# Performance work log

Hardware: AMD Instinct MI355X
Metric: run time of the kernel (lower is better)

Reference implementation:

```python
import jax, jax.numpy as jnp
import numpy as np


def setup_inputs() -> dict:
    key = jax.random.key(0)
    kq, kk, kv = jax.random.split(key, 3)
    B, S, D = 16, 4096, 64
    q = jax.random.normal(kq, (B, S, D), dtype=jnp.float32)
    k = jax.random.normal(kk, (B, S, D), dtype=jnp.float32)
    v = jax.random.normal(kv, (B, S, D), dtype=jnp.float32)
    return {"q": q, "k": k, "v": v}


def reference(q, k, v):
    # scale = 1/sqrt(head_dim), the canonical value passed as `scale` in the repo
    scale = 1.0 / jnp.sqrt(jnp.asarray(q.shape[-1], dtype=q.dtype))
    # scores: [B, Sq, Sk] = q @ k^T  (torch.bmm(q, k.transpose(1,2)))
    scores = jnp.einsum("bqd,bkd->bqk", q, k) * scale
    # softmax over key dim (dim=2); dropout p=0.0 is identity in eval
    attention = jax.nn.softmax(scores, axis=2)
    # context: [B, Sq, D] = attention @ v
    context = jnp.einsum("bqk,bkd->bqd", attention, v)
    return (context, attention)
```

## Files before the change

kernel.cpp:

```cpp
#include <hip/hip_runtime.h>
#include <stdint.h>

typedef _Float16 f16x8 __attribute__((ext_vector_type(8)));
typedef _Float16 f16x4 __attribute__((ext_vector_type(4)));
typedef float    f32x4 __attribute__((ext_vector_type(4)));

#define S_LEN 4096
#define D_DIM 64
#define NB 16
constexpr size_t NE = (size_t)NB * S_LEN * D_DIM;

__global__ __launch_bounds__(256) void k_prep3(const float* __restrict__ k,
                                               _Float16* __restrict__ k3) {
  int g = blockIdx.x * 256 + threadIdx.x;
  int tile = g >> 9, c = g & 511;
  int grp = c >> 6, lane = c & 63;
  int ds = grp >> 2, nf = grp & 3;
  int row = nf * 16 + (lane & 15);
  int d0 = ds * 32 + ((lane >> 4) << 3);
  const float* src = k + ((size_t)tile * 64 + row) * D_DIM + d0;
  f32x4 a = *reinterpret_cast<const f32x4*>(src);
  f32x4 b4 = *reinterpret_cast<const f32x4*>(src + 4);
  f16x8 o;
#pragma unroll
  for (int i = 0; i < 4; ++i) {
    o[i] = (_Float16)a[i];
    o[i + 4] = (_Float16)b4[i];
  }
  *reinterpret_cast<f16x8*>(k3 + (size_t)g * 8) = o;
}

__global__ __launch_bounds__(256) void v_prep3(const float* __restrict__ v,
                                               _Float16* __restrict__ v3) {
  __shared__ float t[64][65];
  int tile = blockIdx.x;
  int c = threadIdx.x & 63, rg = threadIdx.x >> 6;
#pragma unroll
  for (int j = 0; j < 16; ++j)
    t[rg + 4 * j][c] = v[((size_t)tile * 64 + rg + 4 * j) * D_DIM + c];
  __syncthreads();
  _Float16* dst = v3 + (size_t)tile * 4096;
#pragma unroll
  for (int j = 0; j < 4; ++j) {
    int cc = threadIdx.x + 256 * j;
    int g = cc >> 6, lane = cc & 63;
    int nf = g >> 2, dn = g & 3;
    int kl = nf * 16 + ((lane >> 4) << 2);
    int d = dn * 16 + (lane & 15);
    f16x4 o;
#pragma unroll
    for (int i = 0; i < 4; ++i) o[i] = (_Float16)t[kl + i][d];
    *reinterpret_cast<f16x4*>(dst + ((g >> 1) << 9) + lane * 8 + ((g & 1) << 2)) = o;
  }
}

constexpr float CEXP = 0.18033688011112042f;

#define PIPE_BARRIER()                                 \
  do {                                                 \
    asm volatile("s_waitcnt lgkmcnt(0)" ::: "memory"); \
    __builtin_amdgcn_s_barrier();                      \
    __builtin_amdgcn_sched_barrier(0);                 \
  } while (0)

__global__ __launch_bounds__(256, 4) void attn_k(const float* __restrict__ q,
                                                 const _Float16* __restrict__ k3,
                                                 const _Float16* __restrict__ v3,
                                                 float* __restrict__ ctx,
                                                 float* __restrict__ att) {
  __shared__ _Float16 ktile[4][4096];
  const int tid = threadIdx.x, w = tid >> 6, lane = tid & 63;
  const int l15 = lane & 15, lh = lane >> 4;
  const int bid = blockIdx.x;
  const int logical = (bid & 7) * 128 + (bid >> 3);
  const int b = logical >> 6, qt = logical & 63;
  const int qrow = qt * 64 + w * 16 + l15;

  f16x8 qf[2];
#pragma unroll
  for (int ds = 0; ds < 2; ++ds) {
    const float* qp = q + ((size_t)b * S_LEN + qrow) * D_DIM + ds * 32 + 8 * lh;
    f32x4 a = *reinterpret_cast<const f32x4*>(qp);
    f32x4 c4 = *reinterpret_cast<const f32x4*>(qp + 4);
#pragma unroll
    for (int i = 0; i < 4; ++i) {
      qf[ds][i] = (_Float16)(a[i] * CEXP);
      qf[ds][i + 4] = (_Float16)(c4[i] * CEXP);
    }
  }

  const _Float16* k3b = k3 + (size_t)(b * 64) * 4096;

  f16x8 s0, s1, s2, s3;
  auto load2 = [&](int ta, int tb2) {
    const _Float16* sa_ = k3b + (size_t)ta * 4096;
    const _Float16* sb_ = k3b + (size_t)tb2 * 4096;
    s0 = *reinterpret_cast<const f16x8*>(sa_ + tid * 8);
    s1 = *reinterpret_cast<const f16x8*>(sa_ + (tid + 256) * 8);
    s2 = *reinterpret_cast<const f16x8*>(sb_ + tid * 8);
    s3 = *reinterpret_cast<const f16x8*>(sb_ + (tid + 256) * 8);
  };
  auto write2 = [&](int set) {
    *reinterpret_cast<f16x8*>(&ktile[set * 2][tid * 8]) = s0;
    *reinterpret_cast<f16x8*>(&ktile[set * 2][(tid + 256) * 8]) = s1;
    *reinterpret_cast<f16x8*>(&ktile[set * 2 + 1][tid * 8]) = s2;
    *reinterpret_cast<f16x8*>(&ktile[set * 2 + 1][(tid + 256) * 8]) = s3;
  };

  auto qk = [&](int buf, f32x4(&sa)[4]) {
#pragma unroll
    for (int ds = 0; ds < 2; ++ds)
#pragma unroll
      for (int nf = 0; nf < 4; ++nf) {
        const int g = ds * 4 + nf;
        f16x8 kf = *reinterpret_cast<const f16x8*>(&ktile[buf][(g * 64 + lane) * 8]);
        sa[nf] = __builtin_amdgcn_mfma_f32_16x16x32_f16(kf, qf[ds], sa[nf], 0, 0, 0);
      }
  };

  const _Float16* v3b = v3 + (size_t)(b * 64) * 4096 + lane * 8;

  load2(0, 1);
  write2(0);
  PIPE_BARRIER();
  load2(2, 3);
  float ls[4] = {};
  f32x4 ca[4] = {};
  for (int p = 0; p < 32; ++p) {
    const int set = p & 1;
    write2(set ^ 1);
    const int na = 2 * p + 4 < 64 ? 2 * p + 4 : 62;
    load2(na, na + 1);
#pragma unroll
    for (int half = 0; half < 2; ++half) {
      const int t = 2 * p + half;
      const _Float16* vp = v3b + (size_t)t * 4096;
      f16x8 vv8[8];
#pragma unroll
      for (int g2 = 0; g2 < 8; ++g2)
        vv8[g2] = *reinterpret_cast<const f16x8*>(vp + (size_t)g2 * 512);
      f32x4 sa[4] = {};
      __builtin_amdgcn_s_setprio(1);
      qk(set * 2 + half, sa);
      __builtin_amdgcn_s_setprio(0);
      f16x4 pb[4];
#pragma unroll
      for (int nf = 0; nf < 4; ++nf) {
        f32x4 pf;
        pf[0] = exp2f(sa[nf][0]);
        pf[1] = exp2f(sa[nf][1]);
        pf[2] = exp2f(sa[nf][2]);
        pf[3] = exp2f(sa[nf][3]);
        ls[nf] += (pf[0] + pf[1]) + (pf[2] + pf[3]);
        pb[nf][0] = (_Float16)pf[0];
        pb[nf][1] = (_Float16)pf[1];
        pb[nf][2] = (_Float16)pf[2];
        pb[nf][3] = (_Float16)pf[3];
      }
      __builtin_amdgcn_s_setprio(1);
#pragma unroll
      for (int nf = 0; nf < 4; ++nf)
#pragma unroll
        for (int dn = 0; dn < 4; ++dn) {
          const int g = nf * 4 + dn;
          f16x4 vf = (g & 1) ? __builtin_shufflevector(vv8[g >> 1], vv8[g >> 1], 4, 5, 6, 7)
                             : __builtin_shufflevector(vv8[g >> 1], vv8[g >> 1], 0, 1, 2, 3);
          ca[dn] = __builtin_amdgcn_mfma_f32_16x16x16f16(vf, pb[nf], ca[dn], 0, 0, 0);
        }
      __builtin_amdgcn_s_setprio(0);
    }
    PIPE_BARRIER();
  }
  float lsum = (ls[0] + ls[1]) + (ls[2] + ls[3]);
  lsum += __shfl_xor(lsum, 16);
  lsum += __shfl_xor(lsum, 32);
  const float linv = 1.0f / lsum;
  const float lb = -__log2f(lsum);

#pragma unroll
  for (int dn = 0; dn < 4; ++dn) {
    f32x4 co = ca[dn];
    co[0] *= linv; co[1] *= linv; co[2] *= linv; co[3] *= linv;
    *reinterpret_cast<f32x4*>(ctx + ((size_t)b * S_LEN + qrow) * D_DIM + dn * 16 + 4 * lh) = co;
  }

  load2(0, 1);
  write2(0);
  PIPE_BARRIER();
  load2(2, 3);
  float* attrow = att + ((size_t)b * S_LEN + qrow) * S_LEN;
  for (int p = 0; p < 32; ++p) {
    const int set = p & 1;
    write2(set ^ 1);
    const int na = 2 * p + 4 < 64 ? 2 * p + 4 : 62;
    load2(na, na + 1);
#pragma unroll
    for (int half = 0; half < 2; ++half) {
      const int t = 2 * p + half;
      f32x4 sa[4] = {};
      __builtin_amdgcn_s_setprio(1);
      qk(set * 2 + half, sa);
      __builtin_amdgcn_s_setprio(0);
#pragma unroll
      for (int nf = 0; nf < 4; ++nf) {
        f32x4 pf;
        pf[0] = exp2f(sa[nf][0] + lb);
        pf[1] = exp2f(sa[nf][1] + lb);
        pf[2] = exp2f(sa[nf][2] + lb);
        pf[3] = exp2f(sa[nf][3] + lb);
        *reinterpret_cast<f32x4*>(attrow + t * 64 + nf * 16 + 4 * lh) = pf;
      }
    }
    PIPE_BARRIER();
  }
}

extern "C" void kernel_launch(void* const* d_in, const int* in_sizes, int n_in,
                              void* d_out, int out_size, void* d_ws, size_t ws_size,
                              hipStream_t stream) {
  const float* q = (const float*)d_in[0];
  const float* k = (const float*)d_in[1];
  const float* v = (const float*)d_in[2];
  float* ctx = (float*)d_out;
  float* att = ctx + NE;

  _Float16* k3 = (_Float16*)d_ws;
  _Float16* v3 = (_Float16*)((char*)d_ws + 2 * NE);

  k_prep3<<<(int)(NE / 8 / 256), 256, 0, stream>>>(k, k3);
  v_prep3<<<NB * 64, 256, 0, stream>>>(v, v3);
  attn_k<<<1024, 256, 0, stream>>>(q, k3, v3, ctx, att);
}
```

Measured before the change: 397.9 us.

## Process two query tiles per block, fusing A's output pass with B's stats pass

Each block now handles 128 query rows as two tiles. The attention-write pass for the first tile is fused with the softmax-sum and PV pass for the second, sharing the K tile loads and barriers. This removes one of four K sweeps per 128 rows. In exchange the grid is halved, launch bounds allow only 2 blocks per CU, and register pressure rises from holding two Q fragments.

```diff
diff --git a/kernel.cpp b/kernel.cpp
--- a/kernel.cpp
+++ b/kernel.cpp
@@ -63,7 +63,7 @@
     __builtin_amdgcn_sched_barrier(0);                 \
   } while (0)
 
-__global__ __launch_bounds__(256, 4) void attn_k(const float* __restrict__ q,
+__global__ __launch_bounds__(256, 2) void attn_k(const float* __restrict__ q,
                                                  const _Float16* __restrict__ k3,
                                                  const _Float16* __restrict__ v3,
                                                  float* __restrict__ ctx,
@@ -72,24 +72,31 @@
   const int tid = threadIdx.x, w = tid >> 6, lane = tid & 63;
   const int l15 = lane & 15, lh = lane >> 4;
   const int bid = blockIdx.x;
-  const int logical = (bid & 7) * 128 + (bid >> 3);
-  const int b = logical >> 6, qt = logical & 63;
-  const int qrow = qt * 64 + w * 16 + l15;
-
-  f16x8 qf[2];
+  const int logical = (bid & 7) * 64 + (bid >> 3);
+  const int b = logical >> 5, pt = logical & 31;
+  const int qrowA = pt * 128 + w * 16 + l15;
+  const int qrowB = qrowA + 64;
+
+  f16x8 qfA[2], qfB[2];
 #pragma unroll
   for (int ds = 0; ds < 2; ++ds) {
-    const float* qp = q + ((size_t)b * S_LEN + qrow) * D_DIM + ds * 32 + 8 * lh;
-    f32x4 a = *reinterpret_cast<const f32x4*>(qp);
-    f32x4 c4 = *reinterpret_cast<const f32x4*>(qp + 4);
+    const float* qpA = q + ((size_t)b * S_LEN + qrowA) * D_DIM + ds * 32 + 8 * lh;
+    const float* qpB = q + ((size_t)b * S_LEN + qrowB) * D_DIM + ds * 32 + 8 * lh;
+    f32x4 a0 = *reinterpret_cast<const f32x4*>(qpA);
+    f32x4 a1 = *reinterpret_cast<const f32x4*>(qpA + 4);
+    f32x4 b0 = *reinterpret_cast<const f32x4*>(qpB);
+    f32x4 b1 = *reinterpret_cast<const f32x4*>(qpB + 4);
 #pragma unroll
     for (int i = 0; i < 4; ++i) {
-      qf[ds][i] = (_Float16)(a[i] * CEXP);
-      qf[ds][i + 4] = (_Float16)(c4[i] * CEXP);
+      qfA[ds][i] = (_Float16)(a0[i] * CEXP);
+      qfA[ds][i + 4] = (_Float16)(a1[i] * CEXP);
+      qfB[ds][i] = (_Float16)(b0[i] * CEXP);
+      qfB[ds][i + 4] = (_Float16)(b1[i] * CEXP);
     }
   }
 
   const _Float16* k3b = k3 + (size_t)(b * 64) * 4096;
+  const _Float16* v3b = v3 + (size_t)(b * 64) * 4096 + lane * 8;
 
   f16x8 s0, s1, s2, s3;
   auto load2 = [&](int ta, int tb2) {
@@ -107,7 +114,7 @@
     *reinterpret_cast<f16x8*>(&ktile[set * 2 + 1][(tid + 256) * 8]) = s3;
   };
 
-  auto qk = [&](int buf, f32x4(&sa)[4]) {
+  auto qk = [&](int buf, const f16x8(&qf)[2], f32x4(&sa)[4]) {
 #pragma unroll
     for (int ds = 0; ds < 2; ++ds)
 #pragma unroll
@@ -118,7 +125,8 @@
       }
   };
 
-  const _Float16* v3b = v3 + (size_t)(b * 64) * 4096 + lane * 8;
+  float* attrowA = att + ((size_t)b * S_LEN + qrowA) * S_LEN;
+  float* attrowB = att + ((size_t)b * S_LEN + qrowB) * S_LEN;
 
   load2(0, 1);
   write2(0);
@@ -141,7 +149,7 @@
         vv8[g2] = *reinterpret_cast<const f16x8*>(vp + (size_t)g2 * 512);
       f32x4 sa[4] = {};
       __builtin_amdgcn_s_setprio(1);
-      qk(set * 2 + half, sa);
+      qk(set * 2 + half, qfA, sa);
       __builtin_amdgcn_s_setprio(0);
       f16x4 pb[4];
 #pragma unroll
@@ -174,21 +182,23 @@
   float lsum = (ls[0] + ls[1]) + (ls[2] + ls[3]);
   lsum += __shfl_xor(lsum, 16);
   lsum += __shfl_xor(lsum, 32);
-  const float linv = 1.0f / lsum;
-  const float lb = -__log2f(lsum);
-
-#pragma unroll
-  for (int dn = 0; dn < 4; ++dn) {
-    f32x4 co = ca[dn];
-    co[0] *= linv; co[1] *= linv; co[2] *= linv; co[3] *= linv;
-    *reinterpret_cast<f32x4*>(ctx + ((size_t)b * S_LEN + qrow) * D_DIM + dn * 16 + 4 * lh) = co;
-  }
+  {
+    const float linv = 1.0f / lsum;
+#pragma unroll
+    for (int dn = 0; dn < 4; ++dn) {
+      f32x4 co = ca[dn];
+      co[0] *= linv; co[1] *= linv; co[2] *= linv; co[3] *= linv;
+      *reinterpret_cast<f32x4*>(ctx + ((size_t)b * S_LEN + qrowA) * D_DIM + dn * 16 + 4 * lh) = co;
+    }
+  }
+  const float lbA = -__log2f(lsum);
 
   load2(0, 1);
   write2(0);
   PIPE_BARRIER();
   load2(2, 3);
-  float* attrow = att + ((size_t)b * S_LEN + qrow) * S_LEN;
+  ls[0] = ls[1] = ls[2] = ls[3] = 0.f;
+  ca[0] = ca[1] = ca[2] = ca[3] = f32x4{};
   for (int p = 0; p < 32; ++p) {
     const int set = p & 1;
     write2(set ^ 1);
@@ -197,18 +207,95 @@
 #pragma unroll
     for (int half = 0; half < 2; ++half) {
       const int t = 2 * p + half;
+      const int buf = set * 2 + half;
+      const _Float16* vp = v3b + (size_t)t * 4096;
+      f16x8 vv8[8];
+#pragma unroll
+      for (int g2 = 0; g2 < 8; ++g2)
+        vv8[g2] = *reinterpret_cast<const f16x8*>(vp + (size_t)g2 * 512);
+      f32x4 saA[4] = {};
+      __builtin_amdgcn_s_setprio(1);
+      qk(buf, qfA, saA);
+      __builtin_amdgcn_s_setprio(0);
+#pragma unroll
+      for (int nf = 0; nf < 4; ++nf) {
+        f32x4 pf;
+        pf[0] = exp2f(saA[nf][0] + lbA);
+        pf[1] = exp2f(saA[nf][1] + lbA);
+        pf[2] = exp2f(saA[nf][2] + lbA);
+        pf[3] = exp2f(saA[nf][3] + lbA);
+        *reinterpret_cast<f32x4*>(attrowA + t * 64 + nf * 16 + 4 * lh) = pf;
+      }
+      f32x4 saB[4] = {};
+      __builtin_amdgcn_s_setprio(1);
+      qk(buf, qfB, saB);
+      __builtin_amdgcn_s_setprio(0);
+      f16x4 pb[4];
+#pragma unroll
+      for (int nf = 0; nf < 4; ++nf) {
+        f32x4 pf;
+        pf[0] = exp2f(saB[nf][0]);
+        pf[1] = exp2f(saB[nf][1]);
+        pf[2] = exp2f(saB[nf][2]);
+        pf[3] = exp2f(saB[nf][3]);
+        ls[nf] += (pf[0] + pf[1]) + (pf[2] + pf[3]);
+        pb[nf][0] = (_Float16)pf[0];
+        pb[nf][1] = (_Float16)pf[1];
+        pb[nf][2] = (_Float16)pf[2];
+        pb[nf][3] = (_Float16)pf[3];
+      }
+      __builtin_amdgcn_s_setprio(1);
+#pragma unroll
+      for (int nf = 0; nf < 4; ++nf)
+#pragma unroll
+        for (int dn = 0; dn < 4; ++dn) {
+          const int g = nf * 4 + dn;
+          f16x4 vf = (g & 1) ? __builtin_shufflevector(vv8[g >> 1], vv8[g >> 1], 4, 5, 6, 7)
+                             : __builtin_shufflevector(vv8[g >> 1], vv8[g >> 1], 0, 1, 2, 3);
+          ca[dn] = __builtin_amdgcn_mfma_f32_16x16x16f16(vf, pb[nf], ca[dn], 0, 0, 0);
+        }
+      __builtin_amdgcn_s_setprio(0);
+    }
+    PIPE_BARRIER();
+  }
+  lsum = (ls[0] + ls[1]) + (ls[2] + ls[3]);
+  lsum += __shfl_xor(lsum, 16);
+  lsum += __shfl_xor(lsum, 32);
+  {
+    const float linv = 1.0f / lsum;
+#pragma unroll
+    for (int dn = 0; dn < 4; ++dn) {
+      f32x4 co = ca[dn];
+      co[0] *= linv; co[1] *= linv; co[2] *= linv; co[3] *= linv;
+      *reinterpret_cast<f32x4*>(ctx + ((size_t)b * S_LEN + qrowB) * D_DIM + dn * 16 + 4 * lh) = co;
+    }
+  }
+  const float lbB = -__log2f(lsum);
+
+  load2(0, 1);
+  write2(0);
+  PIPE_BARRIER();
+  load2(2, 3);
+  for (int p = 0; p < 32; ++p) {
+    const int set = p & 1;
+    write2(set ^ 1);
+    const int na = 2 * p + 4 < 64 ? 2 * p + 4 : 62;
+    load2(na, na + 1);
+#pragma unroll
+    for (int half = 0; half < 2; ++half) {
+      const int t = 2 * p + half;
       f32x4 sa[4] = {};
       __builtin_amdgcn_s_setprio(1);
-      qk(set * 2 + half, sa);
+      qk(set * 2 + half, qfB, sa);
       __builtin_amdgcn_s_setprio(0);
 #pragma unroll
       for (int nf = 0; nf < 4; ++nf) {
         f32x4 pf;
-        pf[0] = exp2f(sa[nf][0] + lb);
-        pf[1] = exp2f(sa[nf][1] + lb);
-        pf[2] = exp2f(sa[nf][2] + lb);
-        pf[3] = exp2f(sa[nf][3] + lb);
-        *reinterpret_cast<f32x4*>(attrow + t * 64 + nf * 16 + 4 * lh) = pf;
+        pf[0] = exp2f(sa[nf][0] + lbB);
+        pf[1] = exp2f(sa[nf][1] + lbB);
+        pf[2] = exp2f(sa[nf][2] + lbB);
+        pf[3] = exp2f(sa[nf][3] + lbB);
+        *reinterpret_cast<f32x4*>(attrowB + t * 64 + nf * 16 + 4 * lh) = pf;
       }
     }
     PIPE_BARRIER();
@@ -229,5 +316,5 @@
 
   k_prep3<<<(int)(NE / 8 / 256), 256, 0, stream>>>(k, k3);
   v_prep3<<<NB * 64, 256, 0, stream>>>(v, v3);
-  attn_k<<<1024, 256, 0, stream>>>(q, k3, v3, ctx, att);
+  attn_k<<<512, 256, 0, stream>>>(q, k3, v3, ctx, att);
 }
```

Measured after the change: 481.4 us. 1.21x slower.
